# Kernel optimization log

Hardware: AMD Instinct MI355X
Metric: run time of the kernel (lower is better)

The kernel has to match this reference:

```python
import jax, jax.numpy as jnp
import numpy as np

ALPHA = 0.1  # LeakyReLU negative slope
F_OUT = 128

def _leaky(x):
    return jnp.where(x >= 0, x, ALPHA * x)

def setup_inputs() -> dict:
    key = jax.random.key(0)
    ks = jax.random.split(key, 12)
    B, N, F_IN = 4, 4096, 128
    q = jax.random.normal(ks[0], (B, N, F_IN), jnp.float32)
    k = jax.random.normal(ks[1], (B, N, F_IN), jnp.float32)
    v = jax.random.normal(ks[2], (B, N, F_IN), jnp.float32)
    adj = jax.random.randint(ks[3], (B, N, N), 0, 2, jnp.int32)
    s = 1.0 / np.sqrt(F_IN)
    Wq_w = jax.random.uniform(ks[4], (F_OUT, F_IN), jnp.float32, -s, s)
    Wq_b = jax.random.uniform(ks[5], (F_OUT,), jnp.float32, -s, s)
    Wk_w = jax.random.uniform(ks[6], (F_OUT, F_IN), jnp.float32, -s, s)
    Wk_b = jax.random.uniform(ks[7], (F_OUT,), jnp.float32, -s, s)
    Wv_w = jax.random.uniform(ks[8], (F_OUT, F_IN), jnp.float32, -s, s)
    Wv_b = jax.random.uniform(ks[9], (F_OUT,), jnp.float32, -s, s)
    # xavier_uniform with gain=1.414 on (2F,1)
    lim = 1.414 * np.sqrt(6.0 / (2 * F_OUT + 1))
    a = jax.random.uniform(ks[10], (2 * F_OUT, 1), jnp.float32, -lim, lim)
    so = 1.0 / np.sqrt(F_OUT)
    Wo_w = jax.random.uniform(ks[11], (F_OUT, F_OUT), jnp.float32, -so, so)
    return {"q": q, "k": k, "v": v, "adj": adj, "Wq_w": Wq_w, "Wq_b": Wq_b,
            "Wk_w": Wk_w, "Wk_b": Wk_b, "Wv_w": Wv_w, "Wv_b": Wv_b,
            "a": a, "Wo_w": Wo_w}

def reference(q, k, v, adj, Wq_w, Wq_b, Wk_w, Wk_b, Wv_w, Wv_b, a, Wo_w):
    qp = q @ Wq_w.T + Wq_b                      # (B,N,F)
    kp = k @ Wk_w.T + Wk_b
    vp = v @ Wv_w.T + Wv_b
    Wh1 = qp @ a[:F_OUT]                        # (B,N,1)
    Wh2 = kp @ a[F_OUT:]                        # (B,N,1)
    e = _leaky(Wh1 + jnp.swapaxes(Wh2, 1, 2))   # (B,N,N)
    e = jnp.where(adj > 0, e, jnp.float32(-1e9))
    att = jax.nn.softmax(e, axis=-1)
    h = jnp.einsum('bnm,bmf->bnf', att, vp)     # (B,N,F)
    return _leaky(h @ Wo_w.T)
```

## Files before the change

kernel.cpp:

```cpp
#include <hip/hip_runtime.h>


constexpr int B = 4, N = 4096, F = 128;
constexpr int BN = B * N;
constexpr int BK = 64;
#define ALPHA 0.1f

using float4v = __attribute__((ext_vector_type(4))) float;
using short8 = __attribute__((ext_vector_type(8))) short;

__device__ __forceinline__ float leaky(float x) { return x >= 0.f ? x : ALPHA * x; }
__device__ __forceinline__ unsigned short f2bf(float x) {
    unsigned u = __float_as_uint(x);
    u = (u + 0x7FFFu + ((u >> 16) & 1u)) >> 16;
    return (unsigned short)u;
}

__global__ void k_prep(const float* __restrict__ Wq_w, const float* __restrict__ Wq_b,
                       const float* __restrict__ Wk_w, const float* __restrict__ Wk_b,
                       const float* __restrict__ a, float* __restrict__ c1,
                       float* __restrict__ c2, float* __restrict__ d12) {
    __shared__ float as[2 * F];
    __shared__ float red[2 * F];
    int t = threadIdx.x;
    as[t] = a[t];
    __syncthreads();
    int f = t & 127;
    const float* W = (t < F) ? Wq_w : Wk_w;
    const float* ao = (t < F) ? as : as + F;
    float s = 0.f;
#pragma unroll 8
    for (int o = 0; o < F; o++) s = fmaf(W[o * F + f], ao[o], s);
    if (t < F) c1[f] = s; else c2[f] = s;
    red[t] = (t < F) ? Wq_b[f] * as[f] : Wk_b[f] * as[F + f];
    __syncthreads();
    for (int st = 64; st > 0; st >>= 1) {
        if (f < st) red[t] += red[t + st];
        __syncthreads();
    }
    if (t == 0) d12[0] = red[0];
    if (t == F) d12[1] = red[F];
}

__global__ void k_wh(const float* __restrict__ q, const float* __restrict__ k,
                     const float* __restrict__ c1, const float* __restrict__ c2,
                     const float* __restrict__ d12,
                     float* __restrict__ Wh1, float* __restrict__ Wh2) {
    __shared__ float c1s[F], c2s[F];
    int t = threadIdx.x;
    if (t < F) c1s[t] = c1[t]; else c2s[t - F] = c2[t - F];
    __syncthreads();
    int row = blockIdx.x * 8 + (t >> 5);
    int lane = t & 31;
    float4 q4 = reinterpret_cast<const float4*>(q)[row * 32 + lane];
    float4 k4 = reinterpret_cast<const float4*>(k)[row * 32 + lane];
    float s1 = q4.x * c1s[lane * 4 + 0] + q4.y * c1s[lane * 4 + 1] +
               q4.z * c1s[lane * 4 + 2] + q4.w * c1s[lane * 4 + 3];
    float s2 = k4.x * c2s[lane * 4 + 0] + k4.y * c2s[lane * 4 + 1] +
               k4.z * c2s[lane * 4 + 2] + k4.w * c2s[lane * 4 + 3];
    for (int m = 16; m > 0; m >>= 1) { s1 += __shfl_xor(s1, m); s2 += __shfl_xor(s2, m); }
    if (lane == 0) { Wh1[row] = s1 + d12[0]; Wh2[row] = s2 + d12[1]; }
}

__global__ void k_max2(const float* __restrict__ Wh2, float* __restrict__ M2) {
    int b = blockIdx.x, t = threadIdx.x;
    float m = -1e30f;
    for (int i = t; i < N; i += 256) m = fmaxf(m, Wh2[b * N + i]);
    __shared__ float red[256];
    red[t] = m;
    __syncthreads();
    for (int s = 128; s > 0; s >>= 1) { if (t < s) red[t] = fmaxf(red[t], red[t + s]); __syncthreads(); }
    if (t == 0) M2[b] = red[0];
}

__global__ void k_tab(const float* __restrict__ Wh1, const float* __restrict__ Wh2,
                      const float* __restrict__ M2,
                      float* __restrict__ P1, float* __restrict__ Q1,
                      float* __restrict__ P2, float* __restrict__ Q2) {
    int i = blockIdx.x * 256 + threadIdx.x;
    int b = i >> 12;
    float w1 = Wh1[i], w2 = Wh2[i];
    float mi = leaky(w1 + M2[b]);
    P1[i] = __expf(w1 - mi);
    Q1[i] = __expf(ALPHA * w1 - mi);
    P2[i] = __expf(w2);
    Q2[i] = __expf(ALPHA * w2);
}

__global__ __launch_bounds__(256) void k_vp(const float* __restrict__ v,
                                            const float* __restrict__ Wv_w,
                                            const float* __restrict__ Wv_b,
                                            unsigned short* __restrict__ vpT) {
    __shared__ float vs[32][F];
    __shared__ float Ws[F][129];
    __shared__ unsigned short ts[F][40];
    int t = threadIdx.x;
    int row0g = blockIdx.x * 32;
    int b = row0g >> 12;
    int row0 = row0g & (N - 1);
    {
        const float4* src = reinterpret_cast<const float4*>(v + row0g * F);
        float4* dst = reinterpret_cast<float4*>(&vs[0][0]);
#pragma unroll
        for (int u = 0; u < 4; u++) dst[u * 256 + t] = src[u * 256 + t];
    }
    {
        const float4* src = reinterpret_cast<const float4*>(Wv_w);
#pragma unroll
        for (int u = 0; u < 16; u++) {
            int unit = u * 256 + t;
            int r = unit >> 5, s = unit & 31;
            float4 val = src[unit];
            Ws[r][s * 4 + 0] = val.x; Ws[r][s * 4 + 1] = val.y;
            Ws[r][s * 4 + 2] = val.z; Ws[r][s * 4 + 3] = val.w;
        }
    }
    int f = t & 127, g = t >> 7;
    float bias = Wv_b[f];
    __syncthreads();
    float acc[16];
#pragma unroll
    for (int r = 0; r < 16; r++) acc[r] = bias;
    for (int kk = 0; kk < F; kk++) {
        float wk = Ws[f][kk];
#pragma unroll
        for (int r = 0; r < 16; r++) acc[r] = fmaf(vs[g * 16 + r][kk], wk, acc[r]);
    }
#pragma unroll
    for (int r = 0; r < 16; r++) ts[f][g * 16 + r] = f2bf(acc[r]);
    __syncthreads();
    int fr = t >> 1, hseg = t & 1;
    uint4 d0 = *reinterpret_cast<uint4*>(&ts[fr][hseg * 16]);
    uint4 d1 = *reinterpret_cast<uint4*>(&ts[fr][hseg * 16 + 8]);
    unsigned short* dst = vpT + ((size_t)(b * F + fr) * N + row0 + hseg * 16);
    *reinterpret_cast<uint4*>(dst) = d0;
    *reinterpret_cast<uint4*>(dst + 8) = d1;
}

__global__ __launch_bounds__(256) void k_attn(
    const unsigned short* __restrict__ vpT, const int* __restrict__ adj,
    const float* __restrict__ Wh1, const float* __restrict__ P1, const float* __restrict__ Q1,
    const float* __restrict__ P2, const float* __restrict__ Q2, const float* __restrict__ Wh2,
    float* __restrict__ h_part, float* __restrict__ den_part) {
    __shared__ unsigned short bs[F][72];
    __shared__ float P2s[BK], Q2s[BK], W2s[BK];
    int t = threadIdx.x;
    int idx = blockIdx.x;
    int half = idx & 1;
    int tile = (idx >> 1) & 63;
    int b = idx >> 7;
    int i0 = tile * 64;
    int jb0 = half * 2048;
    int widx = t >> 6, lane = t & 63, m = lane & 15, q = lane >> 4;
    int row = i0 + widx * 16 + m;
    int gi = b * N + row;
    float p1 = P1[gi], q1 = Q1[gi], t1 = -Wh1[gi];
    const int* adjr = adj + (long long)gi * N + jb0;
    const unsigned short* vb = vpT + (size_t)b * F * N + jb0;
    const float* P2g = P2 + b * N + jb0;
    const float* Q2g = Q2 + b * N + jb0;
    const float* W2g = Wh2 + b * N + jb0;

    float4v acc[8];
#pragma unroll
    for (int nt = 0; nt < 8; nt++) acc[nt] = (float4v){0.f, 0.f, 0.f, 0.f};
    float den = 0.f;

    for (int j0 = 0; j0 < 2048; j0 += BK) {
        {
#pragma unroll
            for (int u = 0; u < 4; u++) {
                int unit = u * 256 + t;
                int r = unit >> 3, s = unit & 7;
                *reinterpret_cast<uint4*>(&bs[r][s * 8]) =
                    *reinterpret_cast<const uint4*>(vb + (size_t)r * N + j0 + s * 8);
            }
        }
        if (t < 64) P2s[t] = P2g[j0 + t];
        else if (t < 128) Q2s[t - 64] = Q2g[j0 + t - 64];
        else if (t < 192) W2s[t - 128] = W2g[j0 + t - 128];
        __syncthreads();
#pragma unroll
        for (int kh = 0; kh < 2; kh++) {
            int jl = kh * 32 + q * 8;
            int4 a0 = *reinterpret_cast<const int4*>(adjr + j0 + jl);
            int4 a1 = *reinterpret_cast<const int4*>(adjr + j0 + jl + 4);
            float4 p2a = *reinterpret_cast<const float4*>(&P2s[jl]);
            float4 p2b = *reinterpret_cast<const float4*>(&P2s[jl + 4]);
            float4 q2a = *reinterpret_cast<const float4*>(&Q2s[jl]);
            float4 q2b = *reinterpret_cast<const float4*>(&Q2s[jl + 4]);
            float4 x2a = *reinterpret_cast<const float4*>(&W2s[jl]);
            float4 x2b = *reinterpret_cast<const float4*>(&W2s[jl + 4]);
            float w0 = a0.x ? ((x2a.x >= t1) ? p1 * p2a.x : q1 * q2a.x) : 0.f;
            float w1 = a0.y ? ((x2a.y >= t1) ? p1 * p2a.y : q1 * q2a.y) : 0.f;
            float w2 = a0.z ? ((x2a.z >= t1) ? p1 * p2a.z : q1 * q2a.z) : 0.f;
            float w3 = a0.w ? ((x2a.w >= t1) ? p1 * p2a.w : q1 * q2a.w) : 0.f;
            float w4 = a1.x ? ((x2b.x >= t1) ? p1 * p2b.x : q1 * q2b.x) : 0.f;
            float w5 = a1.y ? ((x2b.y >= t1) ? p1 * p2b.y : q1 * q2b.y) : 0.f;
            float w6 = a1.z ? ((x2b.z >= t1) ? p1 * p2b.z : q1 * q2b.z) : 0.f;
            float w7 = a1.w ? ((x2b.w >= t1) ? p1 * p2b.w : q1 * q2b.w) : 0.f;
            den += ((w0 + w1) + (w2 + w3)) + ((w4 + w5) + (w6 + w7));
            short8 af;
            af[0] = (short)f2bf(w0); af[1] = (short)f2bf(w1);
            af[2] = (short)f2bf(w2); af[3] = (short)f2bf(w3);
            af[4] = (short)f2bf(w4); af[5] = (short)f2bf(w5);
            af[6] = (short)f2bf(w6); af[7] = (short)f2bf(w7);
#pragma unroll
            for (int nt = 0; nt < 8; nt++) {
                short8 bf = *reinterpret_cast<const short8*>(&bs[nt * 16 + m][kh * 32 + q * 8]);
                acc[nt] = __builtin_amdgcn_mfma_f32_16x16x32_bf16(af, bf, acc[nt], 0, 0, 0);
            }
        }
        __syncthreads();
    }
    den += __shfl_xor(den, 16);
    den += __shfl_xor(den, 32);
    if (q == 0) atomicAdd(&den_part[gi], den);
    int orow = b * N + i0 + widx * 16 + q * 4;
#pragma unroll
    for (int nt = 0; nt < 8; nt++)
#pragma unroll
        for (int r = 0; r < 4; r++)
            atomicAdd(&h_part[(size_t)(orow + r) * F + nt * 16 + m], acc[nt][r]);
}

__global__ __launch_bounds__(256) void k_out(const float* __restrict__ h_part,
                                             const float* __restrict__ den_part,
                                             const float* __restrict__ Wo_w,
                                             float* __restrict__ out) {
    __shared__ float hs[32][F];
    __shared__ float Ws[F][129];
    int t = threadIdx.x;
    int row0 = blockIdx.x * 32;
    {
        const float4* src = reinterpret_cast<const float4*>(Wo_w);
#pragma unroll
        for (int u = 0; u < 16; u++) {
            int unit = u * 256 + t;
            int r = unit >> 5, s = unit & 31;
            float4 val = src[unit];
            Ws[r][s * 4 + 0] = val.x; Ws[r][s * 4 + 1] = val.y;
            Ws[r][s * 4 + 2] = val.z; Ws[r][s * 4 + 3] = val.w;
        }
    }
#pragma unroll
    for (int u = 0; u < 4; u++) {
        int unit = u * 256 + t;
        int r = unit >> 5, s = unit & 31;
        float4 hv = *reinterpret_cast<const float4*>(h_part + (size_t)(row0 + r) * F + s * 4);
        float inv = 1.f / den_part[row0 + r];
        float4 o = make_float4(hv.x * inv, hv.y * inv, hv.z * inv, hv.w * inv);
        *reinterpret_cast<float4*>(&hs[r][s * 4]) = o;
    }
    __syncthreads();
    int f = t & 127, g = t >> 7;
    float acc[16];
#pragma unroll
    for (int r = 0; r < 16; r++) acc[r] = 0.f;
    for (int kk = 0; kk < F; kk++) {
        float wk = Ws[f][kk];
#pragma unroll
        for (int r = 0; r < 16; r++) acc[r] = fmaf(hs[g * 16 + r][kk], wk, acc[r]);
    }
#pragma unroll
    for (int r = 0; r < 16; r++) out[(size_t)(row0 + g * 16 + r) * F + f] = leaky(acc[r]);
}

extern "C" void kernel_launch(void* const* d_in, const int* in_sizes, int n_in,
                              void* d_out, int out_size, void* d_ws, size_t ws_size,
                              hipStream_t stream) {
    const float* q    = (const float*)d_in[0];
    const float* k    = (const float*)d_in[1];
    const float* v    = (const float*)d_in[2];
    const int*   adj  = (const int*)d_in[3];
    const float* Wq_w = (const float*)d_in[4];
    const float* Wq_b = (const float*)d_in[5];
    const float* Wk_w = (const float*)d_in[6];
    const float* Wk_b = (const float*)d_in[7];
    const float* Wv_w = (const float*)d_in[8];
    const float* Wv_b = (const float*)d_in[9];
    const float* a    = (const float*)d_in[10];
    const float* Wo_w = (const float*)d_in[11];
    float* out = (float*)d_out;
    float* ws = (float*)d_ws;

    unsigned short* vpT = (unsigned short*)ws;
    float* h_part   = ws + BN * F / 2;
    float* den_part = h_part + BN * F;
    float* Wh1 = den_part + BN;
    float* Wh2 = Wh1 + BN;
    float* P1  = Wh2 + BN;
    float* Q1  = P1 + BN;
    float* P2  = Q1 + BN;
    float* Q2  = P2 + BN;
    float* c1  = Q2 + BN;
    float* c2  = c1 + F;
    float* d12 = c2 + F;
    float* M2  = d12 + 2;

    hipMemsetAsync(h_part, 0, (size_t)(BN * F + BN) * sizeof(float), stream);
    k_prep<<<1, 256, 0, stream>>>(Wq_w, Wq_b, Wk_w, Wk_b, a, c1, c2, d12);
    k_wh<<<BN / 8, 256, 0, stream>>>(q, k, c1, c2, d12, Wh1, Wh2);
    k_max2<<<B, 256, 0, stream>>>(Wh2, M2);
    k_tab<<<BN / 256, 256, 0, stream>>>(Wh1, Wh2, M2, P1, Q1, P2, Q2);
    k_vp<<<BN / 32, 256, 0, stream>>>(v, Wv_w, Wv_b, vpT);
    k_attn<<<B * 64 * 2, 256, 0, stream>>>(vpT, adj, Wh1, P1, Q1, P2, Q2, Wh2, h_part, den_part);
    k_out<<<BN / 32, 256, 0, stream>>>(h_part, den_part, Wo_w, out);
}
```

Baseline: 511.3 us.

## Double-buffer attention tiles, prefetch adjacency in registers, replace atomics with split partials

The attention kernel now gives each wave 32 rows instead of 16, so every V tile loaded into shared memory feeds twice as many MFMAs. The next V tile and adjacency chunk are prefetched into registers and written to a second shared buffer while the current one computes. The column-side tables are staged once per block. The column range is split four ways with plain stores to per-split partial buffers, which removes the memset and the float atomics, and k_out sums the four partials. This costs more registers and more partial-buffer traffic in k_out, and packs bf16 pairs with a perm instruction.

```diff
diff --git a/kernel.cpp b/kernel.cpp
--- a/kernel.cpp
+++ b/kernel.cpp
@@ -4,6 +4,9 @@
 constexpr int B = 4, N = 4096, F = 128;
 constexpr int BN = B * N;
 constexpr int BK = 64;
+constexpr int SPLITS = 4;
+constexpr int JC = N / SPLITS;
+constexpr int NIT = JC / BK;
 #define ALPHA 0.1f
 
 using float4v = __attribute__((ext_vector_type(4))) float;
@@ -14,6 +17,12 @@
     unsigned u = __float_as_uint(x);
     u = (u + 0x7FFFu + ((u >> 16) & 1u)) >> 16;
     return (unsigned short)u;
+}
+__device__ __forceinline__ unsigned pack_bf2(float lo, float hi) {
+    unsigned a = __float_as_uint(lo), b2 = __float_as_uint(hi);
+    a = a + 0x7FFFu + ((a >> 16) & 1u);
+    b2 = b2 + 0x7FFFu + ((b2 >> 16) & 1u);
+    return __builtin_amdgcn_perm(b2, a, 0x07060302u);
 }
 
 __global__ void k_prep(const float* __restrict__ Wq_w, const float* __restrict__ Wq_b,
@@ -137,91 +146,146 @@
     *reinterpret_cast<uint4*>(dst + 8) = d1;
 }
 
-__global__ __launch_bounds__(256) void k_attn(
+__global__ __launch_bounds__(256, 2) void k_attn(
     const unsigned short* __restrict__ vpT, const int* __restrict__ adj,
     const float* __restrict__ Wh1, const float* __restrict__ P1, const float* __restrict__ Q1,
     const float* __restrict__ P2, const float* __restrict__ Q2, const float* __restrict__ Wh2,
     float* __restrict__ h_part, float* __restrict__ den_part) {
-    __shared__ unsigned short bs[F][72];
-    __shared__ float P2s[BK], Q2s[BK], W2s[BK];
+    __shared__ __align__(16) unsigned short bs[2][F][72];
+    __shared__ __align__(16) float sP2[JC], sQ2[JC], sW2[JC];
     int t = threadIdx.x;
     int idx = blockIdx.x;
-    int half = idx & 1;
-    int tile = (idx >> 1) & 63;
+    int split = idx & 3;
+    int tile = (idx >> 2) & 31;
     int b = idx >> 7;
-    int i0 = tile * 64;
-    int jb0 = half * 2048;
+    int i0 = tile * 128;
+    int jb0 = split * JC;
     int widx = t >> 6, lane = t & 63, m = lane & 15, q = lane >> 4;
-    int row = i0 + widx * 16 + m;
-    int gi = b * N + row;
-    float p1 = P1[gi], q1 = Q1[gi], t1 = -Wh1[gi];
-    const int* adjr = adj + (long long)gi * N + jb0;
+    int r0 = i0 + widx * 32;
+
+    {
+        reinterpret_cast<float4*>(sP2)[t] = reinterpret_cast<const float4*>(P2 + b * N + jb0)[t];
+        reinterpret_cast<float4*>(sQ2)[t] = reinterpret_cast<const float4*>(Q2 + b * N + jb0)[t];
+        reinterpret_cast<float4*>(sW2)[t] = reinterpret_cast<const float4*>(Wh2 + b * N + jb0)[t];
+    }
+
+    int gi0 = b * N + r0 + m;
+    int gi1 = gi0 + 16;
+    float p1a = P1[gi0], q1a = Q1[gi0], t1a = -Wh1[gi0];
+    float p1b = P1[gi1], q1b = Q1[gi1], t1b = -Wh1[gi1];
+
     const unsigned short* vb = vpT + (size_t)b * F * N + jb0;
-    const float* P2g = P2 + b * N + jb0;
-    const float* Q2g = Q2 + b * N + jb0;
-    const float* W2g = Wh2 + b * N + jb0;
-
-    float4v acc[8];
-#pragma unroll
-    for (int nt = 0; nt < 8; nt++) acc[nt] = (float4v){0.f, 0.f, 0.f, 0.f};
-    float den = 0.f;
-
-    for (int j0 = 0; j0 < 2048; j0 += BK) {
-        {
-#pragma unroll
-            for (int u = 0; u < 4; u++) {
-                int unit = u * 256 + t;
-                int r = unit >> 3, s = unit & 7;
-                *reinterpret_cast<uint4*>(&bs[r][s * 8]) =
-                    *reinterpret_cast<const uint4*>(vb + (size_t)r * N + j0 + s * 8);
+    const int* adjbase = adj + (size_t)gi0 * N + jb0 + q * 8;
+
+    uint4 sreg[4];
+    int4 aregA[8], aregB[8];
+
+    auto load_stage = [&](int it) {
+#pragma unroll
+        for (int u = 0; u < 4; u++) {
+            int unit = u * 256 + t;
+            int r = unit >> 3, s = unit & 7;
+            sreg[u] = *reinterpret_cast<const uint4*>(vb + (size_t)r * N + it * BK + s * 8);
+        }
+    };
+    auto write_stage = [&](int pb) {
+#pragma unroll
+        for (int u = 0; u < 4; u++) {
+            int unit = u * 256 + t;
+            int r = unit >> 3, s = unit & 7;
+            *reinterpret_cast<uint4*>(&bs[pb][r][s * 8]) = sreg[u];
+        }
+    };
+    auto load_adj = [&](int it, int4* ar) {
+#pragma unroll
+        for (int rt = 0; rt < 2; rt++)
+#pragma unroll
+            for (int kh = 0; kh < 2; kh++) {
+                const int* p = adjbase + (size_t)rt * 16 * N + it * BK + kh * 32;
+                ar[(rt * 2 + kh) * 2 + 0] = *reinterpret_cast<const int4*>(p);
+                ar[(rt * 2 + kh) * 2 + 1] = *reinterpret_cast<const int4*>(p + 4);
             }
-        }
-        if (t < 64) P2s[t] = P2g[j0 + t];
-        else if (t < 128) Q2s[t - 64] = Q2g[j0 + t - 64];
-        else if (t < 192) W2s[t - 128] = W2g[j0 + t - 128];
+    };
+
+    float4v acc0[8], acc1[8];
+#pragma unroll
+    for (int nt = 0; nt < 8; nt++) {
+        acc0[nt] = (float4v){0.f, 0.f, 0.f, 0.f};
+        acc1[nt] = (float4v){0.f, 0.f, 0.f, 0.f};
+    }
+    float den0 = 0.f, den1 = 0.f;
+
+    auto gen_af = [&](const int4& a0, const int4& a1, const float4& x2a, const float4& x2b,
+                      const float4& p2a, const float4& p2b, const float4& q2a, const float4& q2b,
+                      float p1, float q1, float t1, float& den) -> short8 {
+        float w0 = a0.x ? ((x2a.x >= t1) ? p1 * p2a.x : q1 * q2a.x) : 0.f;
+        float w1 = a0.y ? ((x2a.y >= t1) ? p1 * p2a.y : q1 * q2a.y) : 0.f;
+        float w2 = a0.z ? ((x2a.z >= t1) ? p1 * p2a.z : q1 * q2a.z) : 0.f;
+        float w3 = a0.w ? ((x2a.w >= t1) ? p1 * p2a.w : q1 * q2a.w) : 0.f;
+        float w4 = a1.x ? ((x2b.x >= t1) ? p1 * p2b.x : q1 * q2b.x) : 0.f;
+        float w5 = a1.y ? ((x2b.y >= t1) ? p1 * p2b.y : q1 * q2b.y) : 0.f;
+        float w6 = a1.z ? ((x2b.z >= t1) ? p1 * p2b.z : q1 * q2b.z) : 0.f;
+        float w7 = a1.w ? ((x2b.w >= t1) ? p1 * p2b.w : q1 * q2b.w) : 0.f;
+        den += ((w0 + w1) + (w2 + w3)) + ((w4 + w5) + (w6 + w7));
+        union { short8 s; uint4 u; } r;
+        r.u.x = pack_bf2(w0, w1); r.u.y = pack_bf2(w2, w3);
+        r.u.z = pack_bf2(w4, w5); r.u.w = pack_bf2(w6, w7);
+        return r.s;
+    };
+
+    auto body = [&](int it, int4* cur, int4* nxt, int pb) {
+        if (it + 1 < NIT) {
+            load_stage(it + 1);
+            load_adj(it + 1, nxt);
+        }
+#pragma unroll
+        for (int kh = 0; kh < 2; kh++) {
+            int jl = it * BK + kh * 32 + q * 8;
+            float4 x2a = *reinterpret_cast<const float4*>(&sW2[jl]);
+            float4 x2b = *reinterpret_cast<const float4*>(&sW2[jl + 4]);
+            float4 p2a = *reinterpret_cast<const float4*>(&sP2[jl]);
+            float4 p2b = *reinterpret_cast<const float4*>(&sP2[jl + 4]);
+            float4 q2a = *reinterpret_cast<const float4*>(&sQ2[jl]);
+            float4 q2b = *reinterpret_cast<const float4*>(&sQ2[jl + 4]);
+            short8 af0 = gen_af(cur[kh * 2 + 0], cur[kh * 2 + 1], x2a, x2b, p2a, p2b, q2a, q2b,
+                                p1a, q1a, t1a, den0);
+            short8 af1 = gen_af(cur[(2 + kh) * 2 + 0], cur[(2 + kh) * 2 + 1], x2a, x2b, p2a, p2b,
+                                q2a, q2b, p1b, q1b, t1b, den1);
+#pragma unroll
+            for (int nt = 0; nt < 8; nt++) {
+                short8 bf = *reinterpret_cast<const short8*>(&bs[pb][nt * 16 + m][kh * 32 + q * 8]);
+                acc0[nt] = __builtin_amdgcn_mfma_f32_16x16x32_bf16(af0, bf, acc0[nt], 0, 0, 0);
+                acc1[nt] = __builtin_amdgcn_mfma_f32_16x16x32_bf16(af1, bf, acc1[nt], 0, 0, 0);
+            }
+        }
+        if (it + 1 < NIT) write_stage(pb ^ 1);
         __syncthreads();
-#pragma unroll
-        for (int kh = 0; kh < 2; kh++) {
-            int jl = kh * 32 + q * 8;
-            int4 a0 = *reinterpret_cast<const int4*>(adjr + j0 + jl);
-            int4 a1 = *reinterpret_cast<const int4*>(adjr + j0 + jl + 4);
-            float4 p2a = *reinterpret_cast<const float4*>(&P2s[jl]);
-            float4 p2b = *reinterpret_cast<const float4*>(&P2s[jl + 4]);
-            float4 q2a = *reinterpret_cast<const float4*>(&Q2s[jl]);
-            float4 q2b = *reinterpret_cast<const float4*>(&Q2s[jl + 4]);
-            float4 x2a = *reinterpret_cast<const float4*>(&W2s[jl]);
-            float4 x2b = *reinterpret_cast<const float4*>(&W2s[jl + 4]);
-            float w0 = a0.x ? ((x2a.x >= t1) ? p1 * p2a.x : q1 * q2a.x) : 0.f;
-            float w1 = a0.y ? ((x2a.y >= t1) ? p1 * p2a.y : q1 * q2a.y) : 0.f;
-            float w2 = a0.z ? ((x2a.z >= t1) ? p1 * p2a.z : q1 * q2a.z) : 0.f;
-            float w3 = a0.w ? ((x2a.w >= t1) ? p1 * p2a.w : q1 * q2a.w) : 0.f;
-            float w4 = a1.x ? ((x2b.x >= t1) ? p1 * p2b.x : q1 * q2b.x) : 0.f;
-            float w5 = a1.y ? ((x2b.y >= t1) ? p1 * p2b.y : q1 * q2b.y) : 0.f;
-            float w6 = a1.z ? ((x2b.z >= t1) ? p1 * p2b.z : q1 * q2b.z) : 0.f;
-            float w7 = a1.w ? ((x2b.w >= t1) ? p1 * p2b.w : q1 * q2b.w) : 0.f;
-            den += ((w0 + w1) + (w2 + w3)) + ((w4 + w5) + (w6 + w7));
-            short8 af;
-            af[0] = (short)f2bf(w0); af[1] = (short)f2bf(w1);
-            af[2] = (short)f2bf(w2); af[3] = (short)f2bf(w3);
-            af[4] = (short)f2bf(w4); af[5] = (short)f2bf(w5);
-            af[6] = (short)f2bf(w6); af[7] = (short)f2bf(w7);
-#pragma unroll
-            for (int nt = 0; nt < 8; nt++) {
-                short8 bf = *reinterpret_cast<const short8*>(&bs[nt * 16 + m][kh * 32 + q * 8]);
-                acc[nt] = __builtin_amdgcn_mfma_f32_16x16x32_bf16(af, bf, acc[nt], 0, 0, 0);
-            }
-        }
-        __syncthreads();
-    }
-    den += __shfl_xor(den, 16);
-    den += __shfl_xor(den, 32);
-    if (q == 0) atomicAdd(&den_part[gi], den);
-    int orow = b * N + i0 + widx * 16 + q * 4;
+    };
+
+    load_stage(0);
+    load_adj(0, aregA);
+    write_stage(0);
+    __syncthreads();
+
+#pragma unroll 1
+    for (int ith = 0; ith < NIT / 2; ith++) {
+        body(ith * 2 + 0, aregA, aregB, 0);
+        body(ith * 2 + 1, aregB, aregA, 1);
+    }
+
+    den0 += __shfl_xor(den0, 16); den0 += __shfl_xor(den0, 32);
+    den1 += __shfl_xor(den1, 16); den1 += __shfl_xor(den1, 32);
+    float* dp = den_part + (size_t)split * BN;
+    if (q == 0) { dp[gi0] = den0; dp[gi1] = den1; }
+    float* hp = h_part + (size_t)split * BN * F;
+    int orow0 = b * N + r0 + q * 4;
 #pragma unroll
     for (int nt = 0; nt < 8; nt++)
 #pragma unroll
-        for (int r = 0; r < 4; r++)
-            atomicAdd(&h_part[(size_t)(orow + r) * F + nt * 16 + m], acc[nt][r]);
+        for (int r = 0; r < 4; r++) {
+            hp[(size_t)(orow0 + r) * F + nt * 16 + m] = acc0[nt][r];
+            hp[(size_t)(orow0 + 16 + r) * F + nt * 16 + m] = acc1[nt][r];
+        }
 }
 
 __global__ __launch_bounds__(256) void k_out(const float* __restrict__ h_part,
@@ -247,10 +311,18 @@
     for (int u = 0; u < 4; u++) {
         int unit = u * 256 + t;
         int r = unit >> 5, s = unit & 31;
-        float4 hv = *reinterpret_cast<const float4*>(h_part + (size_t)(row0 + r) * F + s * 4);
-        float inv = 1.f / den_part[row0 + r];
-        float4 o = make_float4(hv.x * inv, hv.y * inv, hv.z * inv, hv.w * inv);
-        *reinterpret_cast<float4*>(&hs[r][s * 4]) = o;
+        size_t off = (size_t)(row0 + r) * F + s * 4;
+        float4 h0 = *reinterpret_cast<const float4*>(h_part + off);
+        float4 h1 = *reinterpret_cast<const float4*>(h_part + (size_t)BN * F + off);
+        float4 h2 = *reinterpret_cast<const float4*>(h_part + (size_t)2 * BN * F + off);
+        float4 h3 = *reinterpret_cast<const float4*>(h_part + (size_t)3 * BN * F + off);
+        float dsum = den_part[row0 + r] + den_part[BN + row0 + r] +
+                     den_part[2 * BN + row0 + r] + den_part[3 * BN + row0 + r];
+        float inv = 1.f / dsum;
+        hs[r][s * 4 + 0] = (h0.x + h1.x + h2.x + h3.x) * inv;
+        hs[r][s * 4 + 1] = (h0.y + h1.y + h2.y + h3.y) * inv;
+        hs[r][s * 4 + 2] = (h0.z + h1.z + h2.z + h3.z) * inv;
+        hs[r][s * 4 + 3] = (h0.w + h1.w + h2.w + h3.w) * inv;
     }
     __syncthreads();
     int f = t & 127, g = t >> 7;
@@ -286,8 +358,8 @@
 
     unsigned short* vpT = (unsigned short*)ws;
     float* h_part   = ws + BN * F / 2;
-    float* den_part = h_part + BN * F;
-    float* Wh1 = den_part + BN;
+    float* den_part = h_part + (size_t)SPLITS * BN * F;
+    float* Wh1 = den_part + SPLITS * BN;
     float* Wh2 = Wh1 + BN;
     float* P1  = Wh2 + BN;
     float* Q1  = P1 + BN;
@@ -298,12 +370,12 @@
     float* d12 = c2 + F;
     float* M2  = d12 + 2;
 
-    hipMemsetAsync(h_part, 0, (size_t)(BN * F + BN) * sizeof(float), stream);
     k_prep<<<1, 256, 0, stream>>>(Wq_w, Wq_b, Wk_w, Wk_b, a, c1, c2, d12);
     k_wh<<<BN / 8, 256, 0, stream>>>(q, k, c1, c2, d12, Wh1, Wh2);
     k_max2<<<B, 256, 0, stream>>>(Wh2, M2);
     k_tab<<<BN / 256, 256, 0, stream>>>(Wh1, Wh2, M2, P1, Q1, P2, Q2);
     k_vp<<<BN / 32, 256, 0, stream>>>(v, Wv_w, Wv_b, vpT);
-    k_attn<<<B * 64 * 2, 256, 0, stream>>>(vpT, adj, Wh1, P1, Q1, P2, Q2, Wh2, h_part, den_part);
+    k_attn<<<B * 32 * SPLITS, 256, 0, stream>>>(vpT, adj, Wh1, P1, Q1, P2, Q2, Wh2,
+                                                h_part, den_part);
     k_out<<<BN / 32, 256, 0, stream>>>(h_part, den_part, Wo_w, out);
 }
```

New measurement: 508.3 us. Within noise of the previous version (-0.6%).
